# Performance work log

Hardware: AMD Instinct MI355X
Metric: run time of the kernel (lower is better)

The kernel has to match this reference:

```python
import jax, jax.numpy as jnp
import numpy as np

N_NODES = 40000
N_EDGES = 640000
IN_DIM = 128
HID_DIM = 128


def _glorot(key, shape):
    fan_in, fan_out = shape[1], shape[0]
    lim = np.sqrt(6.0 / (fan_in + fan_out))
    return jax.random.uniform(key, shape, jnp.float32, -lim, lim)


def setup_inputs() -> dict:
    key = jax.random.key(0)
    ks = jax.random.split(key, 8)
    x = jax.random.normal(ks[0], (N_NODES, IN_DIM), dtype=jnp.float32)
    edge_index = jax.random.randint(ks[1], (2, N_EDGES), 0, N_NODES, dtype=jnp.int64)
    # SAGEConv params: lin_l (applied to aggregated neighbors, has bias), lin_r (self, no bias)
    W1l = _glorot(ks[2], (HID_DIM, IN_DIM))
    b1l = jnp.zeros((HID_DIM,), jnp.float32)
    W1r = _glorot(ks[3], (HID_DIM, IN_DIM))
    W2l = _glorot(ks[4], (HID_DIM, HID_DIM))
    b2l = jnp.zeros((HID_DIM,), jnp.float32)
    W2r = _glorot(ks[5], (HID_DIM, HID_DIM))
    return {"x": x, "edge_index": edge_index, "W1l": W1l, "b1l": b1l,
            "W1r": W1r, "W2l": W2l, "b2l": b2l, "W2r": W2r}


def _sage_conv(x, src, dst, Wl, bl, Wr):
    # mean aggregation of source features into destination nodes
    msg = x[src]  # [E, D] gather
    agg = jax.ops.segment_sum(msg, dst, num_segments=N_NODES)          # [N, D]
    cnt = jax.ops.segment_sum(jnp.ones_like(dst, jnp.float32), dst,
                              num_segments=N_NODES)                     # [N]
    mean = agg / jnp.maximum(cnt, 1.0)[:, None]
    # out = lin_l(mean_neighbors) + lin_r(x)
    return mean @ Wl.T + bl + x @ Wr.T


def reference(x, edge_index, W1l, b1l, W1r, W2l, b2l, W2r):
    src, dst = edge_index[0], edge_index[1]
    h = jax.nn.relu(_sage_conv(x, src, dst, W1l, b1l, W1r))
    h = jax.nn.relu(_sage_conv(h, src, dst, W2l, b2l, W2r))
    return h
```

## Files before the change

kernel.cpp:

```cpp
#include <hip/hip_runtime.h>
#include <hip/hip_bf16.h>

#define DIM 128
#define NN 40000
#define NE 640000
#define NBLK ((NN + 255) / 256)

typedef __attribute__((ext_vector_type(8))) short s16x8;
typedef __attribute__((ext_vector_type(4))) float f32x4;
typedef __attribute__((ext_vector_type(4))) unsigned short u16x4;
typedef __attribute__((ext_vector_type(4))) unsigned int u32x4;

__device__ __forceinline__ float bf16_lo(unsigned v) { return __uint_as_float(v << 16); }
__device__ __forceinline__ float bf16_hi(unsigned v) { return __uint_as_float(v & 0xffff0000u); }
__device__ __forceinline__ unsigned short f_to_bf16(float f) {
    unsigned u = __float_as_uint(f);
    u += 0x7fffu + ((u >> 16) & 1u);
    return (unsigned short)(u >> 16);
}

__global__ void fill_const_f32(float* __restrict__ out, int n, float v) {
    int i = blockIdx.x * blockDim.x + threadIdx.x;
    if (i < n) out[i] = v;
}

__global__ void zero_ints(int* __restrict__ p, int n) {
    int i = blockIdx.x * blockDim.x + threadIdx.x;
    if (i < n) p[i] = 0;
}

__global__ void cvt_f32_bf16(const float* __restrict__ src,
                             unsigned short* __restrict__ dst, int n4) {
    int i = blockIdx.x * blockDim.x + threadIdx.x;
    if (i >= n4) return;
    f32x4 v = *(const f32x4*)(src + 4 * (size_t)i);
    u16x4 o;
    o.x = f_to_bf16(v.x); o.y = f_to_bf16(v.y);
    o.z = f_to_bf16(v.z); o.w = f_to_bf16(v.w);
    *(u16x4*)(dst + 4 * (size_t)i) = o;
}

__global__ void cvt_weights(const float* __restrict__ w0, const float* __restrict__ w1,
                            const float* __restrict__ w2, const float* __restrict__ w3,
                            unsigned short* __restrict__ dst) {
    int m = blockIdx.y;
    const float* src = (m == 0) ? w0 : (m == 1) ? w1 : (m == 2) ? w2 : w3;
    int i = blockIdx.x * blockDim.x + threadIdx.x;
    f32x4 v = *(const f32x4*)(src + 4 * (size_t)i);
    u16x4 o;
    o.x = f_to_bf16(v.x); o.y = f_to_bf16(v.y);
    o.z = f_to_bf16(v.z); o.w = f_to_bf16(v.w);
    *(u16x4*)(dst + (size_t)m * 16384 + 4 * (size_t)i) = o;
}

__global__ void detect_fmt(const int* __restrict__ ei, int* __restrict__ flag) {
    int lane = threadIdx.x;
    int w = ei[2 * lane + 1];
    unsigned long long m = __ballot(w == 0);
    if (lane == 0) *flag = (m == ~0ull) ? 1 : 0;
}


__global__ void count_deg(const int* __restrict__ ei, const int* __restrict__ fmt,
                          int* __restrict__ deg) {
    int e = blockIdx.x * blockDim.x + threadIdx.x;
    if (e >= NE) return;
    int dst = (*fmt) ? ((const int2*)ei)[NE + e].x : ei[NE + e];
    if ((unsigned)dst < (unsigned)NN) atomicAdd(&deg[dst], 1);
}

__global__ void block_sums(const int* __restrict__ deg, int* __restrict__ bsum) {
    __shared__ int sh[256];
    int i = blockIdx.x * 256 + threadIdx.x;
    sh[threadIdx.x] = (i < NN) ? deg[i] : 0;
    __syncthreads();
    for (int off = 128; off > 0; off >>= 1) {
        if (threadIdx.x < off) sh[threadIdx.x] += sh[threadIdx.x + off];
        __syncthreads();
    }
    if (threadIdx.x == 0) bsum[blockIdx.x] = sh[0];
}

__global__ void scan_bsums(int* __restrict__ bsum, int nb) {
    __shared__ int sh[256];
    int t = threadIdx.x;
    int v = (t < nb) ? bsum[t] : 0;
    sh[t] = v;
    __syncthreads();
    for (int off = 1; off < 256; off <<= 1) {
        int u = (t >= off) ? sh[t - off] : 0;
        __syncthreads();
        sh[t] += u;
        __syncthreads();
    }
    if (t < nb) bsum[t] = sh[t] - v;
}

__global__ void scan_block(const int* __restrict__ deg, const int* __restrict__ bsum,
                           int* __restrict__ row_ptr, int* __restrict__ cursor) {
    __shared__ int sh[256];
    int t = threadIdx.x;
    int i = blockIdx.x * 256 + t;
    int v = (i < NN) ? deg[i] : 0;
    sh[t] = v;
    __syncthreads();
    for (int off = 1; off < 256; off <<= 1) {
        int u = (t >= off) ? sh[t - off] : 0;
        __syncthreads();
        sh[t] += u;
        __syncthreads();
    }
    int excl = sh[t] - v + bsum[blockIdx.x];
    if (i < NN) { row_ptr[i] = excl; cursor[i] = excl; }
    if (i == NN - 1) row_ptr[NN] = excl + v;
}

__global__ void fill_csr(const int* __restrict__ ei, const int* __restrict__ fmt,
                         int* __restrict__ cursor, int* __restrict__ sorted_src) {
    int e = blockIdx.x * blockDim.x + threadIdx.x;
    if (e >= NE) return;
    int src, dst;
    if (*fmt) {
        src = ((const int2*)ei)[e].x;
        dst = ((const int2*)ei)[NE + e].x;
    } else {
        src = ei[e];
        dst = ei[NE + e];
    }
    if ((unsigned)dst >= (unsigned)NN) return;
    int pos = atomicAdd(&cursor[dst], 1);
    if ((unsigned)pos < (unsigned)NE) sorted_src[pos] = src;
}


__global__ void aggregate(const unsigned short* __restrict__ xin,
                          const int* __restrict__ row_ptr,
                          const int* __restrict__ sorted_src,
                          unsigned short* __restrict__ mean_out) {
    int lane = threadIdx.x & 63;
    int wv = threadIdx.x >> 6;
    int n = blockIdx.x * 4 + wv;
    if (n >= NN) return;
    int start = row_ptr[n], end = row_ptr[n + 1];
    int grp = lane >> 4;
    int lid = lane & 15;
    float acc[8] = {0.f, 0.f, 0.f, 0.f, 0.f, 0.f, 0.f, 0.f};
    int i = start + grp;
    for (; i + 4 < end; i += 8) {
        int s1 = sorted_src[i];
        int s2 = sorted_src[i + 4];
        u32x4 v1 = *(const u32x4*)(xin + (size_t)s1 * DIM + lid * 8);
        u32x4 v2 = *(const u32x4*)(xin + (size_t)s2 * DIM + lid * 8);
        acc[0] += bf16_lo(v1.x); acc[1] += bf16_hi(v1.x);
        acc[2] += bf16_lo(v1.y); acc[3] += bf16_hi(v1.y);
        acc[4] += bf16_lo(v1.z); acc[5] += bf16_hi(v1.z);
        acc[6] += bf16_lo(v1.w); acc[7] += bf16_hi(v1.w);
        acc[0] += bf16_lo(v2.x); acc[1] += bf16_hi(v2.x);
        acc[2] += bf16_lo(v2.y); acc[3] += bf16_hi(v2.y);
        acc[4] += bf16_lo(v2.z); acc[5] += bf16_hi(v2.z);
        acc[6] += bf16_lo(v2.w); acc[7] += bf16_hi(v2.w);
    }
    if (i < end) {
        int s = sorted_src[i];
        u32x4 v = *(const u32x4*)(xin + (size_t)s * DIM + lid * 8);
        acc[0] += bf16_lo(v.x); acc[1] += bf16_hi(v.x);
        acc[2] += bf16_lo(v.y); acc[3] += bf16_hi(v.y);
        acc[4] += bf16_lo(v.z); acc[5] += bf16_hi(v.z);
        acc[6] += bf16_lo(v.w); acc[7] += bf16_hi(v.w);
    }
#pragma unroll
    for (int k = 0; k < 8; ++k) {
        acc[k] += __shfl_xor(acc[k], 16, 64);
        acc[k] += __shfl_xor(acc[k], 32, 64);
    }
    if (grp == 0) {
        int d = end - start;
        float inv = 1.f / (float)(d > 1 ? d : 1);
        u32x4 o;
        o.x = (unsigned)f_to_bf16(acc[0] * inv) | ((unsigned)f_to_bf16(acc[1] * inv) << 16);
        o.y = (unsigned)f_to_bf16(acc[2] * inv) | ((unsigned)f_to_bf16(acc[3] * inv) << 16);
        o.z = (unsigned)f_to_bf16(acc[4] * inv) | ((unsigned)f_to_bf16(acc[5] * inv) << 16);
        o.w = (unsigned)f_to_bf16(acc[6] * inv) | ((unsigned)f_to_bf16(acc[7] * inv) << 16);
        *(u32x4*)(mean_out + (size_t)n * DIM + lid * 8) = o;
    }
}


template <bool WRITE_F32>
__global__ __launch_bounds__(256) void sage_gemm(
    const unsigned short* __restrict__ mean,
    const unsigned short* __restrict__ hself,
    const unsigned short* __restrict__ Wl,
    const unsigned short* __restrict__ Wr,
    const float* __restrict__ bias,
    void* __restrict__ outv) {
    int lane = threadIdx.x & 63;
    int wv = threadIdx.x >> 6;
    int quad = lane >> 4;
    int lid = lane & 15;
    int row0 = blockIdx.x * 64;
    int bcol = blockIdx.y * 64 + wv * 16 + lid;

    const unsigned short* wlp = Wl + (size_t)bcol * DIM + quad * 8;
    const unsigned short* wrp = Wr + (size_t)bcol * DIM + quad * 8;
    s16x8 bl[4], br[4];
#pragma unroll
    for (int kb = 0; kb < 4; ++kb) {
        bl[kb] = *(const s16x8*)(wlp + kb * 32);
        br[kb] = *(const s16x8*)(wrp + kb * 32);
    }

    const unsigned short* ap = mean + (size_t)(row0 + lid) * DIM + quad * 8;
    const unsigned short* hp = hself + (size_t)(row0 + lid) * DIM + quad * 8;
    const int TS = 16 * DIM;

    f32x4 acc[4] = {{0,0,0,0},{0,0,0,0},{0,0,0,0},{0,0,0,0}};
    s16x8 am[2][4], ah[2][4];

#pragma unroll
    for (int kb = 0; kb < 4; ++kb) {
        am[0][kb] = *(const s16x8*)(ap + kb * 32);
        ah[0][kb] = *(const s16x8*)(hp + kb * 32);
    }
#pragma unroll
    for (int t = 0; t < 4; ++t) {
        int cb = t & 1, nb = (t + 1) & 1;
        if (t < 3) {
#pragma unroll
            for (int kb = 0; kb < 4; ++kb) {
                am[nb][kb] = *(const s16x8*)(ap + (t + 1) * TS + kb * 32);
                ah[nb][kb] = *(const s16x8*)(hp + (t + 1) * TS + kb * 32);
            }
        }
#pragma unroll
        for (int kb = 0; kb < 4; ++kb)
            acc[t] = __builtin_amdgcn_mfma_f32_16x16x32_bf16(am[cb][kb], bl[kb], acc[t], 0, 0, 0);
#pragma unroll
        for (int kb = 0; kb < 4; ++kb)
            acc[t] = __builtin_amdgcn_mfma_f32_16x16x32_bf16(ah[cb][kb], br[kb], acc[t], 0, 0, 0);
    }

    float bv = bias[bcol];
#pragma unroll
    for (int t = 0; t < 4; ++t) {
#pragma unroll
        for (int r = 0; r < 4; ++r) {
            int orow = row0 + t * 16 + quad * 4 + r;
            float v = fmaxf(acc[t][r] + bv, 0.f);
            if (WRITE_F32)
                ((float*)outv)[(size_t)orow * DIM + bcol] = v;
            else
                ((unsigned short*)outv)[(size_t)orow * DIM + bcol] = f_to_bf16(v);
        }
    }
}


extern "C" void kernel_launch(void* const* d_in, const int* in_sizes, int n_in,
                              void* d_out, int out_size, void* d_ws, size_t ws_size,
                              hipStream_t stream) {
    const float* x   = (const float*)d_in[0];
    const int*   ei  = (const int*)d_in[1];
    const float* W1l = (const float*)d_in[2];
    const float* b1l = (const float*)d_in[3];
    const float* W1r = (const float*)d_in[4];
    const float* W2l = (const float*)d_in[5];
    const float* b2l = (const float*)d_in[6];
    const float* W2r = (const float*)d_in[7];
    float* out = (float*)d_out;

    const int OUT_ELEMS = NN * DIM;

    const size_t OFF_DEG  = 0;
    const size_t OFF_ROW  = 163840;
    const size_t OFF_BSUM = 324608;
    const size_t OFF_CUR  = 327680;
    const size_t OFF_FMT  = 491264;
    const size_t OFF_SRT  = 491520;
    const size_t OFF_WB   = 3051520;
    const size_t OFF_XB   = 3182592;
    const size_t OFF_MEAN = 13422592;
    const size_t OFF_H1   = 23662592;
    const size_t NEEDED   = 33902592;

    if (ws_size < NEEDED) {
        fill_const_f32<<<(OUT_ELEMS + 255) / 256, 256, 0, stream>>>(out, OUT_ELEMS, 50.0f);
        return;
    }

    char* ws = (char*)d_ws;
    int* deg     = (int*)(ws + OFF_DEG);
    int* row_ptr = (int*)(ws + OFF_ROW);
    int* bsum    = (int*)(ws + OFF_BSUM);
    int* cursor  = (int*)(ws + OFF_CUR);
    int* fmtflag = (int*)(ws + OFF_FMT);
    int* sorted  = (int*)(ws + OFF_SRT);
    unsigned short* Wb    = (unsigned short*)(ws + OFF_WB);
    unsigned short* xb    = (unsigned short*)(ws + OFF_XB);
    unsigned short* meanb = (unsigned short*)(ws + OFF_MEAN);
    unsigned short* h1b   = (unsigned short*)(ws + OFF_H1);

    cvt_f32_bf16<<<(OUT_ELEMS / 4 + 255) / 256, 256, 0, stream>>>(x, xb, OUT_ELEMS / 4);
    cvt_weights<<<dim3(16, 4), 256, 0, stream>>>(W1l, W1r, W2l, W2r, Wb);
    unsigned short* W1lb = Wb;
    unsigned short* W1rb = Wb + 16384;
    unsigned short* W2lb = Wb + 32768;
    unsigned short* W2rb = Wb + 49152;

    zero_ints<<<NBLK, 256, 0, stream>>>(deg, NN);
    detect_fmt<<<1, 64, 0, stream>>>(ei, fmtflag);
    count_deg<<<(NE + 255) / 256, 256, 0, stream>>>(ei, fmtflag, deg);
    block_sums<<<NBLK, 256, 0, stream>>>(deg, bsum);
    scan_bsums<<<1, 256, 0, stream>>>(bsum, NBLK);
    scan_block<<<NBLK, 256, 0, stream>>>(deg, bsum, row_ptr, cursor);
    fill_csr<<<(NE + 255) / 256, 256, 0, stream>>>(ei, fmtflag, cursor, sorted);

    aggregate<<<(NN + 3) / 4, 256, 0, stream>>>(xb, row_ptr, sorted, meanb);
    sage_gemm<false><<<dim3(NN / 64, 2), 256, 0, stream>>>(meanb, xb, W1lb, W1rb, b1l, h1b);

    aggregate<<<(NN + 3) / 4, 256, 0, stream>>>(h1b, row_ptr, sorted, meanb);
    sage_gemm<true><<<dim3(NN / 64, 2), 256, 0, stream>>>(meanb, h1b, W2lb, W2rb, b2l, out);
}
```

Before: 253.0 us.

## Fuse neighbor aggregation with SAGE GEMM via shared-memory mean tile

Merges the aggregate and sage_gemm kernels into a single per-layer kernel. Each block computes the mean of 32 nodes into LDS and then runs the MFMA GEMM on that tile, so the mean buffer is never written to or read back from global memory. It also merges the conversion and zero/detect setup kernels to cut launches, and unrolls the gather by four. In exchange, each block now loads the weights itself, and the aggregation loop runs 8 nodes per wave serially, which lowers parallelism and may hide gather latency less well.

```diff
diff --git a/kernel.cpp b/kernel.cpp
--- a/kernel.cpp
+++ b/kernel.cpp
@@ -24,40 +24,40 @@
     if (i < n) out[i] = v;
 }
 
-__global__ void zero_ints(int* __restrict__ p, int n) {
-    int i = blockIdx.x * blockDim.x + threadIdx.x;
-    if (i < n) p[i] = 0;
-}
-
-__global__ void cvt_f32_bf16(const float* __restrict__ src,
-                             unsigned short* __restrict__ dst, int n4) {
-    int i = blockIdx.x * blockDim.x + threadIdx.x;
-    if (i >= n4) return;
-    f32x4 v = *(const f32x4*)(src + 4 * (size_t)i);
+__global__ void cvt_all(const float* __restrict__ x, unsigned short* __restrict__ xb,
+                        const float* __restrict__ w0, const float* __restrict__ w1,
+                        const float* __restrict__ w2, const float* __restrict__ w3,
+                        unsigned short* __restrict__ wb) {
+    int b = blockIdx.x;
+    const float* src;
+    unsigned short* dst;
+    size_t i;
+    if (b < 5000) {
+        src = x; dst = xb;
+        i = (size_t)b * 256 + threadIdx.x;
+    } else {
+        int w = b - 5000;
+        int m = w >> 4;
+        src = (m == 0) ? w0 : (m == 1) ? w1 : (m == 2) ? w2 : w3;
+        dst = wb + (size_t)m * 16384;
+        i = (size_t)(w & 15) * 256 + threadIdx.x;
+    }
+    f32x4 v = *(const f32x4*)(src + 4 * i);
     u16x4 o;
     o.x = f_to_bf16(v.x); o.y = f_to_bf16(v.y);
     o.z = f_to_bf16(v.z); o.w = f_to_bf16(v.w);
-    *(u16x4*)(dst + 4 * (size_t)i) = o;
-}
-
-__global__ void cvt_weights(const float* __restrict__ w0, const float* __restrict__ w1,
-                            const float* __restrict__ w2, const float* __restrict__ w3,
-                            unsigned short* __restrict__ dst) {
-    int m = blockIdx.y;
-    const float* src = (m == 0) ? w0 : (m == 1) ? w1 : (m == 2) ? w2 : w3;
+    *(u16x4*)(dst + 4 * i) = o;
+}
+
+__global__ void zero_detect(int* __restrict__ deg, const int* __restrict__ ei,
+                            int* __restrict__ flag) {
     int i = blockIdx.x * blockDim.x + threadIdx.x;
-    f32x4 v = *(const f32x4*)(src + 4 * (size_t)i);
-    u16x4 o;
-    o.x = f_to_bf16(v.x); o.y = f_to_bf16(v.y);
-    o.z = f_to_bf16(v.z); o.w = f_to_bf16(v.w);
-    *(u16x4*)(dst + (size_t)m * 16384 + 4 * (size_t)i) = o;
-}
-
-__global__ void detect_fmt(const int* __restrict__ ei, int* __restrict__ flag) {
-    int lane = threadIdx.x;
-    int w = ei[2 * lane + 1];
-    unsigned long long m = __ballot(w == 0);
-    if (lane == 0) *flag = (m == ~0ull) ? 1 : 0;
+    if (i < NN) deg[i] = 0;
+    if (blockIdx.x == 0 && threadIdx.x < 64) {
+        int w = ei[2 * threadIdx.x + 1];
+        unsigned long long m = __ballot(w == 0);
+        if (threadIdx.x == 0) *flag = (m == ~0ull) ? 1 : 0;
+    }
 }
 
 
@@ -133,124 +133,112 @@
 }
 
 
-__global__ void aggregate(const unsigned short* __restrict__ xin,
-                          const int* __restrict__ row_ptr,
-                          const int* __restrict__ sorted_src,
-                          unsigned short* __restrict__ mean_out) {
-    int lane = threadIdx.x & 63;
-    int wv = threadIdx.x >> 6;
-    int n = blockIdx.x * 4 + wv;
-    if (n >= NN) return;
-    int start = row_ptr[n], end = row_ptr[n + 1];
-    int grp = lane >> 4;
-    int lid = lane & 15;
-    float acc[8] = {0.f, 0.f, 0.f, 0.f, 0.f, 0.f, 0.f, 0.f};
-    int i = start + grp;
-    for (; i + 4 < end; i += 8) {
-        int s1 = sorted_src[i];
-        int s2 = sorted_src[i + 4];
-        u32x4 v1 = *(const u32x4*)(xin + (size_t)s1 * DIM + lid * 8);
-        u32x4 v2 = *(const u32x4*)(xin + (size_t)s2 * DIM + lid * 8);
-        acc[0] += bf16_lo(v1.x); acc[1] += bf16_hi(v1.x);
-        acc[2] += bf16_lo(v1.y); acc[3] += bf16_hi(v1.y);
-        acc[4] += bf16_lo(v1.z); acc[5] += bf16_hi(v1.z);
-        acc[6] += bf16_lo(v1.w); acc[7] += bf16_hi(v1.w);
-        acc[0] += bf16_lo(v2.x); acc[1] += bf16_hi(v2.x);
-        acc[2] += bf16_lo(v2.y); acc[3] += bf16_hi(v2.y);
-        acc[4] += bf16_lo(v2.z); acc[5] += bf16_hi(v2.z);
-        acc[6] += bf16_lo(v2.w); acc[7] += bf16_hi(v2.w);
-    }
-    if (i < end) {
-        int s = sorted_src[i];
-        u32x4 v = *(const u32x4*)(xin + (size_t)s * DIM + lid * 8);
-        acc[0] += bf16_lo(v.x); acc[1] += bf16_hi(v.x);
-        acc[2] += bf16_lo(v.y); acc[3] += bf16_hi(v.y);
-        acc[4] += bf16_lo(v.z); acc[5] += bf16_hi(v.z);
-        acc[6] += bf16_lo(v.w); acc[7] += bf16_hi(v.w);
-    }
-#pragma unroll
-    for (int k = 0; k < 8; ++k) {
-        acc[k] += __shfl_xor(acc[k], 16, 64);
-        acc[k] += __shfl_xor(acc[k], 32, 64);
-    }
-    if (grp == 0) {
-        int d = end - start;
-        float inv = 1.f / (float)(d > 1 ? d : 1);
-        u32x4 o;
-        o.x = (unsigned)f_to_bf16(acc[0] * inv) | ((unsigned)f_to_bf16(acc[1] * inv) << 16);
-        o.y = (unsigned)f_to_bf16(acc[2] * inv) | ((unsigned)f_to_bf16(acc[3] * inv) << 16);
-        o.z = (unsigned)f_to_bf16(acc[4] * inv) | ((unsigned)f_to_bf16(acc[5] * inv) << 16);
-        o.w = (unsigned)f_to_bf16(acc[6] * inv) | ((unsigned)f_to_bf16(acc[7] * inv) << 16);
-        *(u32x4*)(mean_out + (size_t)n * DIM + lid * 8) = o;
-    }
-}
-
-
 template <bool WRITE_F32>
-__global__ __launch_bounds__(256) void sage_gemm(
-    const unsigned short* __restrict__ mean,
-    const unsigned short* __restrict__ hself,
+__global__ __launch_bounds__(256) void sage_layer(
+    const unsigned short* __restrict__ feat,
+    const int* __restrict__ row_ptr,
+    const int* __restrict__ sorted_src,
     const unsigned short* __restrict__ Wl,
     const unsigned short* __restrict__ Wr,
     const float* __restrict__ bias,
     void* __restrict__ outv) {
+    __shared__ unsigned short smean[32 * DIM];
+
     int lane = threadIdx.x & 63;
     int wv = threadIdx.x >> 6;
-    int quad = lane >> 4;
+    int grp = lane >> 4;
     int lid = lane & 15;
-    int row0 = blockIdx.x * 64;
-    int bcol = blockIdx.y * 64 + wv * 16 + lid;
-
-    const unsigned short* wlp = Wl + (size_t)bcol * DIM + quad * 8;
-    const unsigned short* wrp = Wr + (size_t)bcol * DIM + quad * 8;
-    s16x8 bl[4], br[4];
-#pragma unroll
-    for (int kb = 0; kb < 4; ++kb) {
-        bl[kb] = *(const s16x8*)(wlp + kb * 32);
-        br[kb] = *(const s16x8*)(wrp + kb * 32);
-    }
-
-    const unsigned short* ap = mean + (size_t)(row0 + lid) * DIM + quad * 8;
-    const unsigned short* hp = hself + (size_t)(row0 + lid) * DIM + quad * 8;
-    const int TS = 16 * DIM;
-
-    f32x4 acc[4] = {{0,0,0,0},{0,0,0,0},{0,0,0,0},{0,0,0,0}};
-    s16x8 am[2][4], ah[2][4];
-
-#pragma unroll
-    for (int kb = 0; kb < 4; ++kb) {
-        am[0][kb] = *(const s16x8*)(ap + kb * 32);
-        ah[0][kb] = *(const s16x8*)(hp + kb * 32);
-    }
-#pragma unroll
-    for (int t = 0; t < 4; ++t) {
-        int cb = t & 1, nb = (t + 1) & 1;
-        if (t < 3) {
+    int row0 = blockIdx.x * 32;
+
+    for (int j = 0; j < 8; ++j) {
+        int nl = wv * 8 + j;
+        int n = row0 + nl;
+        int start = row_ptr[n], end = row_ptr[n + 1];
+        float a[8] = {0.f, 0.f, 0.f, 0.f, 0.f, 0.f, 0.f, 0.f};
+        int i = start + grp;
+        for (; i + 12 < end; i += 16) {
+            int s1 = sorted_src[i];
+            int s2 = sorted_src[i + 4];
+            int s3 = sorted_src[i + 8];
+            int s4 = sorted_src[i + 12];
+            u32x4 v1 = *(const u32x4*)(feat + (size_t)s1 * DIM + lid * 8);
+            u32x4 v2 = *(const u32x4*)(feat + (size_t)s2 * DIM + lid * 8);
+            u32x4 v3 = *(const u32x4*)(feat + (size_t)s3 * DIM + lid * 8);
+            u32x4 v4 = *(const u32x4*)(feat + (size_t)s4 * DIM + lid * 8);
+            a[0] += bf16_lo(v1.x) + bf16_lo(v2.x) + bf16_lo(v3.x) + bf16_lo(v4.x);
+            a[1] += bf16_hi(v1.x) + bf16_hi(v2.x) + bf16_hi(v3.x) + bf16_hi(v4.x);
+            a[2] += bf16_lo(v1.y) + bf16_lo(v2.y) + bf16_lo(v3.y) + bf16_lo(v4.y);
+            a[3] += bf16_hi(v1.y) + bf16_hi(v2.y) + bf16_hi(v3.y) + bf16_hi(v4.y);
+            a[4] += bf16_lo(v1.z) + bf16_lo(v2.z) + bf16_lo(v3.z) + bf16_lo(v4.z);
+            a[5] += bf16_hi(v1.z) + bf16_hi(v2.z) + bf16_hi(v3.z) + bf16_hi(v4.z);
+            a[6] += bf16_lo(v1.w) + bf16_lo(v2.w) + bf16_lo(v3.w) + bf16_lo(v4.w);
+            a[7] += bf16_hi(v1.w) + bf16_hi(v2.w) + bf16_hi(v3.w) + bf16_hi(v4.w);
+        }
+        for (; i < end; i += 4) {
+            int s = sorted_src[i];
+            u32x4 v = *(const u32x4*)(feat + (size_t)s * DIM + lid * 8);
+            a[0] += bf16_lo(v.x); a[1] += bf16_hi(v.x);
+            a[2] += bf16_lo(v.y); a[3] += bf16_hi(v.y);
+            a[4] += bf16_lo(v.z); a[5] += bf16_hi(v.z);
+            a[6] += bf16_lo(v.w); a[7] += bf16_hi(v.w);
+        }
+#pragma unroll
+        for (int k = 0; k < 8; ++k) {
+            a[k] += __shfl_xor(a[k], 16, 64);
+            a[k] += __shfl_xor(a[k], 32, 64);
+        }
+        if (grp == 0) {
+            int d = end - start;
+            float inv = 1.f / (float)(d > 1 ? d : 1);
+            u32x4 o;
+            o.x = (unsigned)f_to_bf16(a[0] * inv) | ((unsigned)f_to_bf16(a[1] * inv) << 16);
+            o.y = (unsigned)f_to_bf16(a[2] * inv) | ((unsigned)f_to_bf16(a[3] * inv) << 16);
+            o.z = (unsigned)f_to_bf16(a[4] * inv) | ((unsigned)f_to_bf16(a[5] * inv) << 16);
+            o.w = (unsigned)f_to_bf16(a[6] * inv) | ((unsigned)f_to_bf16(a[7] * inv) << 16);
+            *(u32x4*)(smean + (size_t)nl * DIM + lid * 8) = o;
+        }
+    }
+    __syncthreads();
+
+    int quad = grp;
+#pragma unroll
+    for (int c = 0; c < 2; ++c) {
+        int bcol = c * 64 + wv * 16 + lid;
+        const unsigned short* wl0 = Wl + (size_t)bcol * DIM + quad * 8;
+        const unsigned short* wr0 = Wr + (size_t)bcol * DIM + quad * 8;
+        s16x8 bl[4], br[4];
+#pragma unroll
+        for (int kb = 0; kb < 4; ++kb) {
+            bl[kb] = *(const s16x8*)(wl0 + kb * 32);
+            br[kb] = *(const s16x8*)(wr0 + kb * 32);
+        }
+        float bv = bias[bcol];
+#pragma unroll
+        for (int t = 0; t < 2; ++t) {
+            f32x4 acc = {0.f, 0.f, 0.f, 0.f};
+            const unsigned short* amp = smean + (size_t)(t * 16 + lid) * DIM + quad * 8;
+            const unsigned short* ahp = feat + (size_t)(row0 + t * 16 + lid) * DIM + quad * 8;
+            s16x8 am[4], ah[4];
 #pragma unroll
             for (int kb = 0; kb < 4; ++kb) {
-                am[nb][kb] = *(const s16x8*)(ap + (t + 1) * TS + kb * 32);
-                ah[nb][kb] = *(const s16x8*)(hp + (t + 1) * TS + kb * 32);
+                am[kb] = *(const s16x8*)(amp + kb * 32);
+                ah[kb] = *(const s16x8*)(ahp + kb * 32);
             }
-        }
-#pragma unroll
-        for (int kb = 0; kb < 4; ++kb)
-            acc[t] = __builtin_amdgcn_mfma_f32_16x16x32_bf16(am[cb][kb], bl[kb], acc[t], 0, 0, 0);
-#pragma unroll
-        for (int kb = 0; kb < 4; ++kb)
-            acc[t] = __builtin_amdgcn_mfma_f32_16x16x32_bf16(ah[cb][kb], br[kb], acc[t], 0, 0, 0);
-    }
-
-    float bv = bias[bcol];
-#pragma unroll
-    for (int t = 0; t < 4; ++t) {
-#pragma unroll
-        for (int r = 0; r < 4; ++r) {
-            int orow = row0 + t * 16 + quad * 4 + r;
-            float v = fmaxf(acc[t][r] + bv, 0.f);
-            if (WRITE_F32)
-                ((float*)outv)[(size_t)orow * DIM + bcol] = v;
-            else
-                ((unsigned short*)outv)[(size_t)orow * DIM + bcol] = f_to_bf16(v);
+#pragma unroll
+            for (int kb = 0; kb < 4; ++kb)
+                acc = __builtin_amdgcn_mfma_f32_16x16x32_bf16(am[kb], bl[kb], acc, 0, 0, 0);
+#pragma unroll
+            for (int kb = 0; kb < 4; ++kb)
+                acc = __builtin_amdgcn_mfma_f32_16x16x32_bf16(ah[kb], br[kb], acc, 0, 0, 0);
+#pragma unroll
+            for (int r = 0; r < 4; ++r) {
+                int orow = row0 + t * 16 + quad * 4 + r;
+                float v = fmaxf(acc[r] + bv, 0.f);
+                if (WRITE_F32)
+                    ((float*)outv)[(size_t)orow * DIM + bcol] = v;
+                else
+                    ((unsigned short*)outv)[(size_t)orow * DIM + bcol] = f_to_bf16(v);
+            }
         }
     }
 }
@@ -279,9 +267,8 @@
     const size_t OFF_SRT  = 491520;
     const size_t OFF_WB   = 3051520;
     const size_t OFF_XB   = 3182592;
-    const size_t OFF_MEAN = 13422592;
-    const size_t OFF_H1   = 23662592;
-    const size_t NEEDED   = 33902592;
+    const size_t OFF_H1   = 13422592;
+    const size_t NEEDED   = 23662592;
 
     if (ws_size < NEEDED) {
         fill_const_f32<<<(OUT_ELEMS + 255) / 256, 256, 0, stream>>>(out, OUT_ELEMS, 50.0f);
@@ -295,29 +282,24 @@
     int* cursor  = (int*)(ws + OFF_CUR);
     int* fmtflag = (int*)(ws + OFF_FMT);
     int* sorted  = (int*)(ws + OFF_SRT);
-    unsigned short* Wb    = (unsigned short*)(ws + OFF_WB);
-    unsigned short* xb    = (unsigned short*)(ws + OFF_XB);
-    unsigned short* meanb = (unsigned short*)(ws + OFF_MEAN);
-    unsigned short* h1b   = (unsigned short*)(ws + OFF_H1);
-
-    cvt_f32_bf16<<<(OUT_ELEMS / 4 + 255) / 256, 256, 0, stream>>>(x, xb, OUT_ELEMS / 4);
-    cvt_weights<<<dim3(16, 4), 256, 0, stream>>>(W1l, W1r, W2l, W2r, Wb);
+    unsigned short* Wb  = (unsigned short*)(ws + OFF_WB);
+    unsigned short* xb  = (unsigned short*)(ws + OFF_XB);
+    unsigned short* h1b = (unsigned short*)(ws + OFF_H1);
     unsigned short* W1lb = Wb;
     unsigned short* W1rb = Wb + 16384;
     unsigned short* W2lb = Wb + 32768;
     unsigned short* W2rb = Wb + 49152;
 
-    zero_ints<<<NBLK, 256, 0, stream>>>(deg, NN);
-    detect_fmt<<<1, 64, 0, stream>>>(ei, fmtflag);
+    cvt_all<<<5064, 256, 0, stream>>>(x, xb, W1l, W1r, W2l, W2r, Wb);
+
+    zero_detect<<<NBLK, 256, 0, stream>>>(deg, ei, fmtflag);
     count_deg<<<(NE + 255) / 256, 256, 0, stream>>>(ei, fmtflag, deg);
     block_sums<<<NBLK, 256, 0, stream>>>(deg, bsum);
     scan_bsums<<<1, 256, 0, stream>>>(bsum, NBLK);
     scan_block<<<NBLK, 256, 0, stream>>>(deg, bsum, row_ptr, cursor);
     fill_csr<<<(NE + 255) / 256, 256, 0, stream>>>(ei, fmtflag, cursor, sorted);
 
-    aggregate<<<(NN + 3) / 4, 256, 0, stream>>>(xb, row_ptr, sorted, meanb);
-    sage_gemm<false><<<dim3(NN / 64, 2), 256, 0, stream>>>(meanb, xb, W1lb, W1rb, b1l, h1b);
-
-    aggregate<<<(NN + 3) / 4, 256, 0, stream>>>(h1b, row_ptr, sorted, meanb);
-    sage_gemm<true><<<dim3(NN / 64, 2), 256, 0, stream>>>(meanb, h1b, W2lb, W2rb, b2l, out);
-}
+    sage_layer<false><<<NN / 32, 256, 0, stream>>>(xb, row_ptr, sorted, W1lb, W1rb, b1l, h1b);
+
+    sage_layer<true><<<NN / 32, 256, 0, stream>>>(h1b, row_ptr, sorted, W2lb, W2rb, b2l, out);
+}
```

Measured after the change: 275.9 us. 9.1% more time.
